# Kernel optimization log

Hardware: AMD Instinct MI355X
Metric: run time of the kernel (lower is better)

Reference implementation:

```python
import jax, jax.numpy as jnp
import numpy as np
from jax import lax

D_MODEL = 512
D_STATE = 16
D_CONV = 4
EXPAND = 2
D_INNER = EXPAND * D_MODEL
DT_RANK = (D_MODEL + 15) // 16  # 32


def _mamba_dir(x, in_w, conv_w, conv_b, xproj_w, dt_w, dt_b, A_log, D, out_w):
    # x: (B, L, d_model)
    B, L, _ = x.shape
    xz = jnp.einsum('bld,ed->ble', x, in_w)          # (B, L, 2*d_inner)
    xi, z = jnp.split(xz, 2, axis=-1)                # each (B, L, d_inner)
    # causal depthwise conv over time
    xc = xi.transpose(0, 2, 1)                       # (B, d_inner, L)
    xc = lax.conv_general_dilated(
        xc, conv_w, window_strides=(1,), padding=[(D_CONV - 1, 0)],
        feature_group_count=D_INNER, dimension_numbers=('NCH', 'OIH', 'NCH'))
    xi = jax.nn.silu(xc + conv_b[None, :, None]).transpose(0, 2, 1)  # (B, L, d_inner)
    # input-dependent SSM params
    x_dbl = jnp.einsum('bld,ed->ble', xi, xproj_w)   # (B, L, dt_rank + 2*d_state)
    dt, Bc, Cc = jnp.split(x_dbl, [DT_RANK, DT_RANK + D_STATE], axis=-1)
    delta = jax.nn.softplus(jnp.einsum('blr,dr->bld', dt, dt_w) + dt_b)  # (B, L, d_inner)
    A = -jnp.exp(A_log)                              # (d_inner, d_state)
    deltaA = jnp.exp(delta[..., None] * A)           # (B, L, d_inner, d_state)
    dBx = delta[..., None] * Bc[:, :, None, :] * xi[..., None]  # (B, L, d_inner, d_state)

    def step(h, inputs):
        dA_t, dBx_t, C_t = inputs
        h = dA_t * h + dBx_t                         # (B, d_inner, d_state)
        y = jnp.einsum('bdn,bn->bd', h, C_t)
        return h, y

    h0 = jnp.zeros((B, D_INNER, D_STATE), dtype=x.dtype)
    _, ys = lax.scan(step, h0,
                     (deltaA.transpose(1, 0, 2, 3),
                      dBx.transpose(1, 0, 2, 3),
                      Cc.transpose(1, 0, 2)))
    y = ys.transpose(1, 0, 2)                        # (B, L, d_inner)
    y = y + xi * D
    y = y * jax.nn.silu(z)
    return jnp.einsum('ble,de->bld', y, out_w)       # (B, L, d_model)


def _forward(x, f_in_w, f_conv_w, f_conv_b, f_xproj_w, f_dt_w, f_dt_b, f_A_log, f_D, f_out_w,
             b_in_w, b_conv_w, b_conv_b, b_xproj_w, b_dt_w, b_dt_b, b_A_log, b_D, b_out_w,
             fusion_w, fusion_b, ln_g, ln_b):
    out_fwd = _mamba_dir(x, f_in_w, f_conv_w, f_conv_b, f_xproj_w, f_dt_w, f_dt_b, f_A_log, f_D, f_out_w)
    x_flip = jnp.flip(x, axis=1)
    out_bwd = _mamba_dir(x_flip, b_in_w, b_conv_w, b_conv_b, b_xproj_w, b_dt_w, b_dt_b, b_A_log, b_D, b_out_w)
    out_bwd = jnp.flip(out_bwd, axis=1)
    fused = jnp.concatenate([out_fwd, out_bwd], axis=-1)     # (B, L, 2*d_model)
    out = jnp.einsum('blf,df->bld', fused, fusion_w) + fusion_b
    r = x + out
    mu = jnp.mean(r, axis=-1, keepdims=True)
    var = jnp.var(r, axis=-1, keepdims=True)
    return (r - mu) * lax.rsqrt(var + 1e-5) * ln_g + ln_b


def _mamba_params(key):
    ks = jax.random.split(key, 6)
    s = 0.02
    in_w = jax.random.normal(ks[0], (2 * D_INNER, D_MODEL), jnp.float32) * s
    conv_w = jax.random.normal(ks[1], (D_INNER, 1, D_CONV), jnp.float32) * 0.2
    conv_b = jnp.zeros((D_INNER,), jnp.float32)
    xproj_w = jax.random.normal(ks[2], (DT_RANK + 2 * D_STATE, D_INNER), jnp.float32) * s
    dt_w = jax.random.normal(ks[3], (D_INNER, DT_RANK), jnp.float32) * (DT_RANK ** -0.5)
    dt_b = jax.random.uniform(ks[4], (D_INNER,), jnp.float32, -4.0, -2.0)
    A_log = jnp.log(jnp.broadcast_to(jnp.arange(1, D_STATE + 1, dtype=jnp.float32), (D_INNER, D_STATE)))
    D = jnp.ones((D_INNER,), jnp.float32)
    out_w = jax.random.normal(ks[5], (D_MODEL, D_INNER), jnp.float32) * s
    return in_w, conv_w, conv_b, xproj_w, dt_w, dt_b, A_log, D, out_w


def setup_inputs() -> dict:
    key = jax.random.key(0)
    kx, kf, kb, k1, k2 = jax.random.split(key, 5)
    B, L = 2, 1024
    x = jax.random.normal(kx, (B, L, D_MODEL), jnp.float32)
    f = _mamba_params(kf)
    b = _mamba_params(kb)
    fusion_w = jax.random.normal(k1, (D_MODEL, 2 * D_MODEL), jnp.float32) * 0.02
    fusion_b = jnp.zeros((D_MODEL,), jnp.float32)
    ln_g = jnp.ones((D_MODEL,), jnp.float32)
    ln_b = jnp.zeros((D_MODEL,), jnp.float32)
    names_f = ['f_in_w', 'f_conv_w', 'f_conv_b', 'f_xproj_w', 'f_dt_w', 'f_dt_b', 'f_A_log', 'f_D', 'f_out_w']
    names_b = ['b_in_w', 'b_conv_w', 'b_conv_b', 'b_xproj_w', 'b_dt_w', 'b_dt_b', 'b_A_log', 'b_D', 'b_out_w']
    d = {'x': x, 'fusion_w': fusion_w, 'fusion_b': fusion_b, 'ln_g': ln_g, 'ln_b': ln_b}
    d.update(dict(zip(names_f, f)))
    d.update(dict(zip(names_b, b)))
    return d


def reference(x, f_in_w, f_conv_w, f_conv_b, f_xproj_w, f_dt_w, f_dt_b, f_A_log, f_D, f_out_w,
              b_in_w, b_conv_w, b_conv_b, b_xproj_w, b_dt_w, b_dt_b, b_A_log, b_D, b_out_w,
              fusion_w, fusion_b, ln_g, ln_b):
    return _forward(x, f_in_w, f_conv_w, f_conv_b, f_xproj_w, f_dt_w, f_dt_b, f_A_log, f_D, f_out_w,
                    b_in_w, b_conv_w, b_conv_b, b_xproj_w, b_dt_w, b_dt_b, b_A_log, b_D, b_out_w,
                    fusion_w, fusion_b, ln_g, ln_b)
```

## Files before the change

### kernel.cpp

```cpp
#include <hip/hip_runtime.h>
#include <hip/hip_bf16.h>

typedef __bf16 bf16x8 __attribute__((ext_vector_type(8)));
typedef __bf16 bf16x4 __attribute__((ext_vector_type(4)));
typedef float  f32x4  __attribute__((ext_vector_type(4)));

#define LOG2E 1.44269504088896340f

static __device__ __forceinline__ unsigned short f2bf_bits(float f) {
  unsigned u = __builtin_bit_cast(unsigned, f);
  u = u + 0x7FFFu + ((u >> 16) & 1u);
  return (unsigned short)(u >> 16);
}
static __device__ __forceinline__ __bf16 to_bf16(float f) {
  unsigned short s = f2bf_bits(f);
  return __builtin_bit_cast(__bf16, s);
}
static __device__ __forceinline__ float fast_sigmoid(float x) {
  return __builtin_amdgcn_rcpf(1.f + __builtin_amdgcn_exp2f(-LOG2E * x));
}
static __device__ __forceinline__ float softplus_f(float x) {
  float m = fmaxf(x, 0.f);
  float e = __builtin_amdgcn_exp2f(-LOG2E * fabsf(x));
  return fmaf(__builtin_amdgcn_logf(1.f + e), 1.f / LOG2E, m);
}

struct CastSeg { const float* src; __bf16* dst; int n4; };
struct CastArgs { CastSeg s[8]; };

__global__ __launch_bounds__(256) void cast_kernel(CastArgs a) {
  CastSeg seg = a.s[blockIdx.y];
  int idx = blockIdx.x * 256 + threadIdx.x;
  int stride = gridDim.x * 256;
  const float4* src = (const float4*)seg.src;
  bf16x4* dst = (bf16x4*)seg.dst;
  for (int i = idx; i < seg.n4; i += stride) {
    float4 v = src[i];
    bf16x4 o;
    o[0] = to_bf16(v.x); o[1] = to_bf16(v.y);
    o[2] = to_bf16(v.z); o[3] = to_bf16(v.w);
    dst[i] = o;
  }
}

#define LOADK(AF, BF, kk)                                              \
  do {                                                                 \
    _Pragma("unroll")                                                  \
    for (int mi = 0; mi < MI; ++mi)                                    \
      AF[mi] = *(const bf16x8*)(Ap + (size_t)(mi * 16) * K + (kk));    \
    _Pragma("unroll")                                                  \
    for (int ni = 0; ni < 4; ++ni)                                     \
      BF[ni] = *(const bf16x8*)(Bp[ni] + (kk));                        \
  } while (0)

#define MFMAK(AF, BF)                                                  \
  do {                                                                 \
    _Pragma("unroll")                                                  \
    for (int mi = 0; mi < MI; ++mi)                                    \
      _Pragma("unroll")                                                \
      for (int ni = 0; ni < 4; ++ni)                                   \
        acc[mi][ni] = __builtin_amdgcn_mfma_f32_16x16x32_bf16(         \
            AF[mi], BF[ni], acc[mi][ni], 0, 0, 0);                     \
  } while (0)

template<typename OutT, bool BIAS, bool RESID, bool SPLIT, int MI>
__global__ __launch_bounds__(256) void gemm_bt(
    const __bf16* __restrict__ A, long long sAz,
    const __bf16* __restrict__ B0, const __bf16* __restrict__ B1,
    OutT* __restrict__ C, long long sCz, int ldc,
    int N, int K,
    const float* __restrict__ bias, const float* __restrict__ resid, int ldr,
    __bf16* __restrict__ xiout, __bf16* __restrict__ gateout, long long sXz)
{
  const __bf16* B = (blockIdx.z == 0) ? B0 : B1;
  A += (size_t)blockIdx.z * (size_t)sAz;
  C += (size_t)blockIdx.z * (size_t)sCz;
  if (SPLIT) {
    xiout   += (size_t)blockIdx.z * (size_t)sXz;
    gateout += (size_t)blockIdx.z * (size_t)sXz;
  }
  int lane = threadIdx.x & 63;
  int wid  = threadIdx.x >> 6;
  int rowBase = blockIdx.y * (MI * 32) + (wid >> 1) * (MI * 16);
  int colBase = blockIdx.x * 128 + (wid & 1) * 64;
  int lr = lane & 15;
  int lk = (lane >> 4) << 3;
  const __bf16* Ap = A + (size_t)(rowBase + lr) * K + lk;
  const __bf16* Bp[4];
  #pragma unroll
  for (int ni = 0; ni < 4; ++ni) {
    int br = colBase + ni * 16 + lr;
    if (br > N - 1) br = N - 1;
    Bp[ni] = B + (size_t)br * K + lk;
  }
  f32x4 acc[MI][4] = {};
  bf16x8 aF0[MI], bF0[4], aF1[MI], bF1[4];
  LOADK(aF0, bF0, 0);
  for (int k = 0; k < K; k += 64) {
    LOADK(aF1, bF1, k + 32);
    MFMAK(aF0, bF0);
    if (k + 64 < K) LOADK(aF0, bF0, k + 64);
    MFMAK(aF1, bF1);
  }
  int crow = rowBase + ((lane >> 4) << 2);
  int ccol = colBase + lr;
  #pragma unroll
  for (int mi = 0; mi < MI; ++mi) {
    #pragma unroll
    for (int ni = 0; ni < 4; ++ni) {
      int c = ccol + ni * 16;
      if (c < N) {
        #pragma unroll
        for (int j = 0; j < 4; ++j) {
          int r = crow + mi * 16 + j;
          float v = acc[mi][ni][j];
          if (SPLIT) {
            if (c < 1024) xiout[(size_t)r * 1024 + c] = to_bf16(v);
            else          gateout[(size_t)r * 1024 + (c - 1024)] =
                              to_bf16(v * fast_sigmoid(v));
          } else {
            if (BIAS)  v += bias[c];
            if (RESID) v += resid[(size_t)r * ldr + c];
            if constexpr (sizeof(OutT) == 2) C[(size_t)r * ldc + c] = to_bf16(v);
            else                             C[(size_t)r * ldc + c] = v;
          }
        }
      }
    }
  }
}

#define CT 16
__global__ __launch_bounds__(256) void conv_silu_kernel(
    const __bf16* __restrict__ xiraw,
    const float* __restrict__ f_cw, const float* __restrict__ f_cb,
    const float* __restrict__ b_cw, const float* __restrict__ b_cb,
    __bf16* __restrict__ xi16)
{
  int d  = blockIdx.x * 256 + threadIdx.x;
  int t0 = blockIdx.y * CT;
  int dir = blockIdx.z >> 1, b = blockIdx.z & 1;
  const float* cw = dir ? b_cw : f_cw;
  const float* cb = dir ? b_cb : f_cb;
  float w0 = cw[d*4+0], w1 = cw[d*4+1], w2 = cw[d*4+2], w3 = cw[d*4+3];
  float bias = cb[d];
  size_t rowBase = (size_t)dir * 2048 + (size_t)b * 1024;
  const __bf16* xp = xiraw + rowBase * 1024 + d;
  __bf16* o16 = xi16 + rowBase * 1024 + d;
  float xv[CT + 3];
  if (dir == 0) {
    #pragma unroll
    for (int j = 0; j < CT + 3; ++j) {
      int t = t0 - 3 + j;
      xv[j] = (t >= 0) ? (float)xp[(size_t)t * 1024] : 0.f;
    }
    #pragma unroll
    for (int j = 0; j < CT; ++j) {
      int t = t0 + j;
      float v = fmaf(w0, xv[j], fmaf(w1, xv[j+1], fmaf(w2, xv[j+2], fmaf(w3, xv[j+3], bias))));
      float s = v * fast_sigmoid(v);
      o16[(size_t)t * 1024] = to_bf16(s);
    }
  } else {
    #pragma unroll
    for (int j = 0; j < CT + 3; ++j) {
      int t = t0 + j;
      xv[j] = (t < 1024) ? (float)xp[(size_t)t * 1024] : 0.f;
    }
    #pragma unroll
    for (int j = 0; j < CT; ++j) {
      int t = t0 + j;
      float v = fmaf(w3, xv[j], fmaf(w2, xv[j+1], fmaf(w1, xv[j+2], fmaf(w0, xv[j+3], bias))));
      float s = v * fast_sigmoid(v);
      o16[(size_t)t * 1024] = to_bf16(s);
    }
  }
}

__global__ __launch_bounds__(256) void g2_kernel(
    const __bf16* __restrict__ A,
    const __bf16* __restrict__ B0, const __bf16* __restrict__ B1,
    float* __restrict__ partial)
{
  int slice = blockIdx.x;
  int mt = blockIdx.y;
  int dir = blockIdx.z;
  const __bf16* B = dir ? B1 : B0;
  const __bf16* Ad = A + (size_t)dir * 2048 * 1024;
  int lane = threadIdx.x & 63, wid = threadIdx.x >> 6;
  int rowBase = mt * 64 + wid * 16;
  int lr = lane & 15, lk = (lane >> 4) << 3;
  int k0 = slice * 256;
  const __bf16* Ap = Ad + (size_t)(rowBase + lr) * 1024 + k0 + lk;
  const __bf16* Bp[4];
  #pragma unroll
  for (int ni = 0; ni < 4; ++ni)
    Bp[ni] = B + (size_t)(ni * 16 + lr) * 1024 + k0 + lk;
  f32x4 acc[4] = {};
  #pragma unroll
  for (int k = 0; k < 256; k += 32) {
    bf16x8 aF = *(const bf16x8*)(Ap + k);
    #pragma unroll
    for (int ni = 0; ni < 4; ++ni) {
      bf16x8 bF = *(const bf16x8*)(Bp[ni] + k);
      acc[ni] = __builtin_amdgcn_mfma_f32_16x16x32_bf16(aF, bF, acc[ni], 0, 0, 0);
    }
  }
  int crow = rowBase + ((lane >> 4) << 2);
  float* out = partial + ((size_t)dir * 4 + slice) * 2048 * 64;
  #pragma unroll
  for (int ni = 0; ni < 4; ++ni)
    #pragma unroll
    for (int j = 0; j < 4; ++j)
      out[(size_t)(crow + j) * 64 + ni * 16 + lr] = acc[ni][j];
}

__global__ __launch_bounds__(256) void g2red_kernel(
    const float4* __restrict__ partial, float4* __restrict__ xdbl)
{
  int idx = blockIdx.x * 256 + threadIdx.x;
  int dir = idx >> 15;
  int rest = idx & 32767;
  const float4* p = partial + (size_t)dir * 4 * 32768 + rest;
  float4 a = p[0], b = p[32768], c = p[2 * 32768], d = p[3 * 32768];
  float4 s;
  s.x = a.x + b.x + c.x + d.x;
  s.y = a.y + b.y + c.y + d.y;
  s.z = a.z + b.z + c.z + d.z;
  s.w = a.w + b.w + c.w + d.w;
  xdbl[idx] = s;
}

__global__ __launch_bounds__(256) void delta_kernel(
    const float* __restrict__ xdbl,
    const float* __restrict__ f_dtw, const float* __restrict__ f_dtb,
    const float* __restrict__ b_dtw, const float* __restrict__ b_dtb,
    __bf16* __restrict__ delta16)
{
  int d = blockIdx.x * 256 + threadIdx.x;
  int dir = blockIdx.z;
  const float* dtw = (dir ? b_dtw : f_dtw) + d * 32;
  float w[32];
  #pragma unroll
  for (int k = 0; k < 32; ++k) w[k] = dtw[k];
  float dtb = (dir ? b_dtb : f_dtb)[d];
  int row0 = dir * 2048 + blockIdx.y * 16;
  #pragma unroll
  for (int r = 0; r < 16; ++r) {
    int row = row0 + r;
    const float* xr = xdbl + (size_t)row * 64;
    float acc = dtb;
    #pragma unroll
    for (int k = 0; k < 32; ++k) acc = fmaf(w[k], xr[k], acc);
    delta16[(size_t)row * 1024 + d] = to_bf16(softplus_f(acc));
  }
}

#define NC 64
#define CL 16

__global__ __launch_bounds__(256) void scan_part1(
    const __bf16* __restrict__ delta16, const __bf16* __restrict__ xi16,
    const float* __restrict__ xdbl,
    const float* __restrict__ f_Alog, const float* __restrict__ b_Alog,
    float4* __restrict__ aProd, float4* __restrict__ hPart)
{
  int d = blockIdx.x * 256 + threadIdx.x;
  int g = blockIdx.y;
  int zb = blockIdx.z;
  int dir = zb >> 1, b = zb & 1;
  const float* Alog = (dir ? b_Alog : f_Alog) + d * 16;
  float As[16];
  #pragma unroll
  for (int n = 0; n < 16; ++n)
    As[n] = -__builtin_amdgcn_exp2f(LOG2E * Alog[n]) * LOG2E;
  int base = dir * 2048 + b * 1024;
  float h[16], A[16];
  #pragma unroll
  for (int n = 0; n < 16; ++n) { h[n] = 0.f; A[n] = 1.f; }
  #pragma unroll
  for (int j = 0; j < CL; ++j) {
    int tau = g * CL + j;
    int row = base + (dir ? (1023 - tau) : tau);
    const float* xr = xdbl + (size_t)row * 64;
    float del = (float)delta16[(size_t)row * 1024 + d];
    float xi  = (float)xi16[(size_t)row * 1024 + d];
    float dx = del * xi;
    #pragma unroll
    for (int n = 0; n < 16; ++n) {
      float dA = __builtin_amdgcn_exp2f(del * As[n]);
      h[n] = fmaf(dA, h[n], dx * xr[32 + n]);
      A[n] *= dA;
    }
  }
  size_t o = (((size_t)zb * NC + g) * 1024 + d) * 4;
  #pragma unroll
  for (int q = 0; q < 4; ++q) {
    aProd[o + q] = float4{A[q*4+0], A[q*4+1], A[q*4+2], A[q*4+3]};
    hPart[o + q] = float4{h[q*4+0], h[q*4+1], h[q*4+2], h[q*4+3]};
  }
}

__global__ __launch_bounds__(256) void scan_combine(
    const float* __restrict__ aProd, const float* __restrict__ hPart,
    float* __restrict__ hIn)
{
  int idx = blockIdx.x * 256 + threadIdx.x;
  int zb = idx >> 14;
  int dn = idx & 16383;
  float H = 0.f;
  #pragma unroll 8
  for (int g = 0; g < NC; ++g) {
    size_t o = ((size_t)zb * NC + g) * 16384 + dn;
    float a = aProd[o];
    float hp = hPart[o];
    hIn[o] = H;
    H = fmaf(a, H, hp);
  }
}

__global__ __launch_bounds__(256) void scan_part3(
    const __bf16* __restrict__ delta16, const __bf16* __restrict__ xi16,
    const float* __restrict__ xdbl,
    const __bf16* __restrict__ gatebf,
    const float* __restrict__ f_Alog, const float* __restrict__ b_Alog,
    const float* __restrict__ f_D, const float* __restrict__ b_D,
    const float* __restrict__ hIn,
    __bf16* __restrict__ yout)
{
  int d = blockIdx.x * 256 + threadIdx.x;
  int g = blockIdx.y;
  int zb = blockIdx.z;
  int dir = zb >> 1, b = zb & 1;
  float Dv = (dir ? b_D : f_D)[d];
  const float* Alog = (dir ? b_Alog : f_Alog) + d * 16;
  float As[16];
  #pragma unroll
  for (int n = 0; n < 16; ++n)
    As[n] = -__builtin_amdgcn_exp2f(LOG2E * Alog[n]) * LOG2E;
  float h[16];
  const float4* hi4 = (const float4*)(hIn + (((size_t)zb * NC + g) * 1024 + d) * 16);
  #pragma unroll
  for (int q = 0; q < 4; ++q) {
    float4 hv = hi4[q];
    h[q*4+0] = hv.x; h[q*4+1] = hv.y; h[q*4+2] = hv.z; h[q*4+3] = hv.w;
  }
  int base = dir * 2048 + b * 1024;
  #pragma unroll
  for (int j = 0; j < CL; ++j) {
    int tau = g * CL + j;
    int row = base + (dir ? (1023 - tau) : tau);
    const float* xr = xdbl + (size_t)row * 64;
    float del = (float)delta16[(size_t)row * 1024 + d];
    float xi  = (float)xi16[(size_t)row * 1024 + d];
    float dx = del * xi;
    float ps = 0.f;
    #pragma unroll
    for (int n = 0; n < 16; ++n) {
      float dA = __builtin_amdgcn_exp2f(del * As[n]);
      h[n] = fmaf(dA, h[n], dx * xr[32 + n]);
      ps = fmaf(h[n], xr[48 + n], ps);
    }
    float gate = (float)gatebf[(size_t)row * 1024 + d];
    float y = fmaf(xi, Dv, ps) * gate;
    yout[(size_t)row * 1024 + d] = to_bf16(y);
  }
}

__global__ __launch_bounds__(256) void ln_kernel(
    const float* __restrict__ r, const float* __restrict__ g,
    const float* __restrict__ beta, float* __restrict__ out)
{
  int row = blockIdx.x;
  int tid = threadIdx.x;
  const float* rp = r + (size_t)row * 512;
  float v0 = rp[tid], v1 = rp[tid + 256];
  float s = v0 + v1;
  float q = fmaf(v0, v0, v1 * v1);
  #pragma unroll
  for (int m = 1; m < 64; m <<= 1) {
    s += __shfl_xor(s, m, 64);
    q += __shfl_xor(q, m, 64);
  }
  __shared__ float ls[4], lq[4];
  int wid = tid >> 6;
  if ((tid & 63) == 0) { ls[wid] = s; lq[wid] = q; }
  __syncthreads();
  s = ls[0] + ls[1] + ls[2] + ls[3];
  q = lq[0] + lq[1] + lq[2] + lq[3];
  float mu = s * (1.f / 512.f);
  float var = q * (1.f / 512.f) - mu * mu;
  float rs = rsqrtf(var + 1e-5f);
  float* op = out + (size_t)row * 512;
  op[tid]       = (v0 - mu) * rs * g[tid]       + beta[tid];
  op[tid + 256] = (v1 - mu) * rs * g[tid + 256] + beta[tid + 256];
}

extern "C" void kernel_launch(void* const* d_in, const int* in_sizes, int n_in,
                              void* d_out, int out_size, void* d_ws, size_t ws_size,
                              hipStream_t stream)
{
  const float* x        = (const float*)d_in[0];
  const float* fusion_w = (const float*)d_in[1];
  const float* fusion_b = (const float*)d_in[2];
  const float* ln_g     = (const float*)d_in[3];
  const float* ln_b     = (const float*)d_in[4];
  const float* f_in_w   = (const float*)d_in[5];
  const float* f_conv_w = (const float*)d_in[6];
  const float* f_conv_b = (const float*)d_in[7];
  const float* f_xproj  = (const float*)d_in[8];
  const float* f_dt_w   = (const float*)d_in[9];
  const float* f_dt_b   = (const float*)d_in[10];
  const float* f_A_log  = (const float*)d_in[11];
  const float* f_D      = (const float*)d_in[12];
  const float* f_out_w  = (const float*)d_in[13];
  const float* b_in_w   = (const float*)d_in[14];
  const float* b_conv_w = (const float*)d_in[15];
  const float* b_conv_b = (const float*)d_in[16];
  const float* b_xproj  = (const float*)d_in[17];
  const float* b_dt_w   = (const float*)d_in[18];
  const float* b_dt_b   = (const float*)d_in[19];
  const float* b_A_log  = (const float*)d_in[20];
  const float* b_D      = (const float*)d_in[21];
  const float* b_out_w  = (const float*)d_in[22];

  char* w = (char*)d_ws;
  auto alloc = [&](size_t bytes) -> char* {
    char* p = w;
    w += (bytes + 255) & ~(size_t)255;
    return p;
  };
  __bf16* xbf    = (__bf16*)alloc((size_t)2048 * 512 * 2);
  __bf16* wInF   = (__bf16*)alloc((size_t)2048 * 512 * 2);
  __bf16* wInB   = (__bf16*)alloc((size_t)2048 * 512 * 2);
  __bf16* xprF   = (__bf16*)alloc((size_t)64 * 1024 * 2);
  __bf16* xprB   = (__bf16*)alloc((size_t)64 * 1024 * 2);
  __bf16* wOutF  = (__bf16*)alloc((size_t)512 * 1024 * 2);
  __bf16* wOutB  = (__bf16*)alloc((size_t)512 * 1024 * 2);
  __bf16* wFus   = (__bf16*)alloc((size_t)512 * 1024 * 2);
  __bf16* xiraw  = (__bf16*)alloc((size_t)2 * 2048 * 1024 * 2);
  __bf16* gatebf = (__bf16*)alloc((size_t)2 * 2048 * 1024 * 2);
  __bf16* xi16   = (__bf16*)alloc((size_t)2 * 2048 * 1024 * 2);
  float*  part2  = (float*)alloc((size_t)2 * 4 * 2048 * 64 * 4);
  float*  xdbl   = (float*)alloc((size_t)2 * 2048 * 64 * 4);
  __bf16* delta16= (__bf16*)alloc((size_t)2 * 2048 * 1024 * 2);
  __bf16* ybf    = (__bf16*)alloc((size_t)2 * 2048 * 1024 * 2);
  __bf16* fin    = (__bf16*)alloc((size_t)2048 * 1024 * 2);
  float*  rbuf   = (float*)alloc((size_t)2048 * 512 * 4);
  float*  aProd  = (float*)alloc((size_t)4 * NC * 16384 * 4);
  float*  hPart  = (float*)alloc((size_t)4 * NC * 16384 * 4);
  float*  hInB   = (float*)alloc((size_t)4 * NC * 16384 * 4);
  (void)ws_size; (void)n_in; (void)in_sizes; (void)out_size;

  CastArgs ca;
  ca.s[0] = { x,        xbf,   (2048 * 512) / 4 };
  ca.s[1] = { f_in_w,   wInF,  (2048 * 512) / 4 };
  ca.s[2] = { b_in_w,   wInB,  (2048 * 512) / 4 };
  ca.s[3] = { f_xproj,  xprF,  (64 * 1024) / 4 };
  ca.s[4] = { b_xproj,  xprB,  (64 * 1024) / 4 };
  ca.s[5] = { f_out_w,  wOutF, (512 * 1024) / 4 };
  ca.s[6] = { b_out_w,  wOutB, (512 * 1024) / 4 };
  ca.s[7] = { fusion_w, wFus,  (512 * 1024) / 4 };
  cast_kernel<<<dim3(256, 8), 256, 0, stream>>>(ca);

  gemm_bt<float, false, false, true, 2><<<dim3(16, 32, 2), 256, 0, stream>>>(
      xbf, 0LL, wInF, wInB, (float*)nullptr, 0LL, 0, 2048, 512,
      nullptr, nullptr, 0, xiraw, gatebf, (long long)2048 * 1024);

  conv_silu_kernel<<<dim3(4, 1024 / CT, 4), 256, 0, stream>>>(
      xiraw, f_conv_w, f_conv_b, b_conv_w, b_conv_b, xi16);

  g2_kernel<<<dim3(4, 32, 2), 256, 0, stream>>>(xi16, xprF, xprB, part2);
  g2red_kernel<<<dim3(256), 256, 0, stream>>>((const float4*)part2, (float4*)xdbl);

  delta_kernel<<<dim3(4, 128, 2), 256, 0, stream>>>(
      xdbl, f_dt_w, f_dt_b, b_dt_w, b_dt_b, delta16);

  scan_part1<<<dim3(4, NC, 4), 256, 0, stream>>>(
      delta16, xi16, xdbl, f_A_log, b_A_log, (float4*)aProd, (float4*)hPart);
  scan_combine<<<dim3(256), 256, 0, stream>>>(aProd, hPart, hInB);
  scan_part3<<<dim3(4, NC, 4), 256, 0, stream>>>(
      delta16, xi16, xdbl, gatebf, f_A_log, b_A_log, f_D, b_D, hInB, ybf);

  gemm_bt<__bf16, false, false, false, 2><<<dim3(4, 32, 2), 256, 0, stream>>>(
      ybf, (long long)2048 * 1024, wOutF, wOutB, fin, 512LL, 1024, 512, 1024,
      nullptr, nullptr, 0, nullptr, nullptr, 0LL);

  gemm_bt<float, true, true, false, 2><<<dim3(4, 32, 1), 256, 0, stream>>>(
      fin, 0LL, wFus, wFus, rbuf, 0LL, 512, 512, 1024,
      fusion_b, x, 512, nullptr, nullptr, 0LL);

  ln_kernel<<<2048, 256, 0, stream>>>(rbuf, ln_g, ln_b, (float*)d_out);
}
```

Baseline: 292.0 us.

## Use LDS-staged double-buffered 128x128 GEMM for the input projection

Adds a new GEMM kernel that stages 128x128 A and B tiles through padded, double-buffered shared memory, in place of each wave loading its MFMA fragments straight from global memory. It is used for the input projection (2048x2048x512 per direction), with the grid changed to 128-row tiles. The aim is to cut redundant global and L2 traffic by sharing tiles across waves. In exchange it adds a block barrier every k-step, uses more LDS, and halves the number of blocks. The SPLIT epilogue moves out of the old gemm_bt template into the new kernel.

```diff
diff --git a/kernel.cpp b/kernel.cpp
--- a/kernel.cpp
+++ b/kernel.cpp
@@ -43,6 +43,101 @@
   }
 }
 
+#define LDSTRIDE 40
+template<typename OutT, bool BIAS, bool RESID, bool SPLIT>
+__global__ __launch_bounds__(256) void gemm_lds(
+    const __bf16* __restrict__ A, long long sAz,
+    const __bf16* __restrict__ B0, const __bf16* __restrict__ B1,
+    OutT* __restrict__ C, long long sCz, int ldc,
+    int N, int K,
+    const float* __restrict__ bias, const float* __restrict__ resid, int ldr,
+    __bf16* __restrict__ xiout, __bf16* __restrict__ gateout, long long sXz)
+{
+  __shared__ __bf16 ldsA[2][128 * LDSTRIDE];
+  __shared__ __bf16 ldsB[2][128 * LDSTRIDE];
+  const __bf16* B = (blockIdx.z == 0) ? B0 : B1;
+  A += (size_t)blockIdx.z * (size_t)sAz;
+  C += (size_t)blockIdx.z * (size_t)sCz;
+  if (SPLIT) {
+    xiout   += (size_t)blockIdx.z * (size_t)sXz;
+    gateout += (size_t)blockIdx.z * (size_t)sXz;
+  }
+  int tid = threadIdx.x;
+  int lane = tid & 63, wid = tid >> 6;
+  int wr = wid >> 1, wc = wid & 1;
+  int rowTile = blockIdx.y * 128;
+  int colTile = blockIdx.x * 128;
+  int srow = tid >> 2;
+  int scol = (tid & 3) << 3;
+  const __bf16* Ag  = A + (size_t)(rowTile + srow) * K + scol;
+  const __bf16* Ag2 = Ag + (size_t)64 * K;
+  const __bf16* Bg  = B + (size_t)(colTile + srow) * K + scol;
+  const __bf16* Bg2 = Bg + (size_t)64 * K;
+  int sidx = srow * LDSTRIDE + scol;
+
+  auto stageTo = [&](int buf, int k0) {
+    bf16x8 a0 = *(const bf16x8*)(Ag + k0);
+    bf16x8 a1 = *(const bf16x8*)(Ag2 + k0);
+    bf16x8 b0 = *(const bf16x8*)(Bg + k0);
+    bf16x8 b1 = *(const bf16x8*)(Bg2 + k0);
+    *(bf16x8*)&ldsA[buf][sidx] = a0;
+    *(bf16x8*)&ldsA[buf][64 * LDSTRIDE + sidx] = a1;
+    *(bf16x8*)&ldsB[buf][sidx] = b0;
+    *(bf16x8*)&ldsB[buf][64 * LDSTRIDE + sidx] = b1;
+  };
+
+  int lr = lane & 15;
+  int lk = (lane >> 4) << 3;
+  int aoff = (wr * 64 + lr) * LDSTRIDE + lk;
+  int boff = (wc * 64 + lr) * LDSTRIDE + lk;
+
+  f32x4 acc[4][4] = {};
+  int nSteps = K >> 5;
+  stageTo(0, 0);
+  __syncthreads();
+  for (int ks = 0; ks < nSteps; ++ks) {
+    int cur = ks & 1;
+    if (ks + 1 < nSteps) stageTo(cur ^ 1, (ks + 1) << 5);
+    bf16x8 aF[4], bF[4];
+    #pragma unroll
+    for (int mi = 0; mi < 4; ++mi)
+      aF[mi] = *(const bf16x8*)&ldsA[cur][aoff + mi * 16 * LDSTRIDE];
+    #pragma unroll
+    for (int ni = 0; ni < 4; ++ni)
+      bF[ni] = *(const bf16x8*)&ldsB[cur][boff + ni * 16 * LDSTRIDE];
+    #pragma unroll
+    for (int mi = 0; mi < 4; ++mi)
+      #pragma unroll
+      for (int ni = 0; ni < 4; ++ni)
+        acc[mi][ni] = __builtin_amdgcn_mfma_f32_16x16x32_bf16(aF[mi], bF[ni], acc[mi][ni], 0, 0, 0);
+    __syncthreads();
+  }
+  int crow = rowTile + wr * 64 + ((lane >> 4) << 2);
+  int ccol = colTile + wc * 64 + lr;
+  #pragma unroll
+  for (int mi = 0; mi < 4; ++mi) {
+    #pragma unroll
+    for (int ni = 0; ni < 4; ++ni) {
+      int c = ccol + ni * 16;
+      #pragma unroll
+      for (int j = 0; j < 4; ++j) {
+        int r = crow + mi * 16 + j;
+        float v = acc[mi][ni][j];
+        if (SPLIT) {
+          if (c < 1024) xiout[(size_t)r * 1024 + c] = to_bf16(v);
+          else          gateout[(size_t)r * 1024 + (c - 1024)] =
+                            to_bf16(v * fast_sigmoid(v));
+        } else {
+          if (BIAS)  v += bias[c];
+          if (RESID) v += resid[(size_t)r * ldr + c];
+          if constexpr (sizeof(OutT) == 2) C[(size_t)r * ldc + c] = to_bf16(v);
+          else                             C[(size_t)r * ldc + c] = v;
+        }
+      }
+    }
+  }
+}
+
 #define LOADK(AF, BF, kk)                                              \
   do {                                                                 \
     _Pragma("unroll")                                                  \
@@ -63,22 +158,17 @@
             AF[mi], BF[ni], acc[mi][ni], 0, 0, 0);                     \
   } while (0)
 
-template<typename OutT, bool BIAS, bool RESID, bool SPLIT, int MI>
+template<typename OutT, bool BIAS, bool RESID, int MI>
 __global__ __launch_bounds__(256) void gemm_bt(
     const __bf16* __restrict__ A, long long sAz,
     const __bf16* __restrict__ B0, const __bf16* __restrict__ B1,
     OutT* __restrict__ C, long long sCz, int ldc,
     int N, int K,
-    const float* __restrict__ bias, const float* __restrict__ resid, int ldr,
-    __bf16* __restrict__ xiout, __bf16* __restrict__ gateout, long long sXz)
+    const float* __restrict__ bias, const float* __restrict__ resid, int ldr)
 {
   const __bf16* B = (blockIdx.z == 0) ? B0 : B1;
   A += (size_t)blockIdx.z * (size_t)sAz;
   C += (size_t)blockIdx.z * (size_t)sCz;
-  if (SPLIT) {
-    xiout   += (size_t)blockIdx.z * (size_t)sXz;
-    gateout += (size_t)blockIdx.z * (size_t)sXz;
-  }
   int lane = threadIdx.x & 63;
   int wid  = threadIdx.x >> 6;
   int rowBase = blockIdx.y * (MI * 32) + (wid >> 1) * (MI * 16);
@@ -114,16 +204,10 @@
         for (int j = 0; j < 4; ++j) {
           int r = crow + mi * 16 + j;
           float v = acc[mi][ni][j];
-          if (SPLIT) {
-            if (c < 1024) xiout[(size_t)r * 1024 + c] = to_bf16(v);
-            else          gateout[(size_t)r * 1024 + (c - 1024)] =
-                              to_bf16(v * fast_sigmoid(v));
-          } else {
-            if (BIAS)  v += bias[c];
-            if (RESID) v += resid[(size_t)r * ldr + c];
-            if constexpr (sizeof(OutT) == 2) C[(size_t)r * ldc + c] = to_bf16(v);
-            else                             C[(size_t)r * ldc + c] = v;
-          }
+          if (BIAS)  v += bias[c];
+          if (RESID) v += resid[(size_t)r * ldr + c];
+          if constexpr (sizeof(OutT) == 2) C[(size_t)r * ldc + c] = to_bf16(v);
+          else                             C[(size_t)r * ldc + c] = v;
         }
       }
     }
@@ -463,7 +547,7 @@
   ca.s[7] = { fusion_w, wFus,  (512 * 1024) / 4 };
   cast_kernel<<<dim3(256, 8), 256, 0, stream>>>(ca);
 
-  gemm_bt<float, false, false, true, 2><<<dim3(16, 32, 2), 256, 0, stream>>>(
+  gemm_lds<float, false, false, true><<<dim3(16, 16, 2), 256, 0, stream>>>(
       xbf, 0LL, wInF, wInB, (float*)nullptr, 0LL, 0, 2048, 512,
       nullptr, nullptr, 0, xiraw, gatebf, (long long)2048 * 1024);
 
@@ -482,13 +566,13 @@
   scan_part3<<<dim3(4, NC, 4), 256, 0, stream>>>(
       delta16, xi16, xdbl, gatebf, f_A_log, b_A_log, f_D, b_D, hInB, ybf);
 
-  gemm_bt<__bf16, false, false, false, 2><<<dim3(4, 32, 2), 256, 0, stream>>>(
+  gemm_bt<__bf16, false, false, 2><<<dim3(4, 32, 2), 256, 0, stream>>>(
       ybf, (long long)2048 * 1024, wOutF, wOutB, fin, 512LL, 1024, 512, 1024,
-      nullptr, nullptr, 0, nullptr, nullptr, 0LL);
-
-  gemm_bt<float, true, true, false, 2><<<dim3(4, 32, 1), 256, 0, stream>>>(
+      nullptr, nullptr, 0);
+
+  gemm_bt<float, true, true, 2><<<dim3(4, 32, 1), 256, 0, stream>>>(
       fin, 0LL, wFus, wFus, rbuf, 0LL, 512, 512, 1024,
-      fusion_b, x, 512, nullptr, nullptr, 0LL);
+      fusion_b, x, 512);
 
   ln_kernel<<<2048, 256, 0, stream>>>(rbuf, ln_g, ln_b, (float*)d_out);
 }
```

Measured after the change: 262.8 us. -10.0%, faster.
